# Kernel optimization log

Measured on AMD Instinct MI355X. Metric: run time of the kernel, lower is better.

Reference implementation:

```python
import jax, jax.numpy as jnp
import numpy as np

BIT = 64
M_MARGIN = 2.0 * BIT  # m = 2 * bit
ALPHA = 0.1
N_TRAIN = 100000
N_CLASSES = 100
BATCH = 512


def setup_inputs() -> dict:
    key = jax.random.key(0)
    k1, k2, k3, k4 = jax.random.split(key, 4)
    u = jax.random.normal(k1, (BATCH, BIT), dtype=jnp.float32)
    y = jax.random.randint(k2, (BATCH, N_CLASSES), 0, 2).astype(jnp.float32)
    ind = jnp.arange(BATCH, dtype=jnp.int32)
    U = jax.random.normal(k3, (N_TRAIN, BIT), dtype=jnp.float32)
    Y = jax.random.randint(k4, (N_TRAIN, N_CLASSES), 0, 2).astype(jnp.float32)
    return {"u": u, "y": y, "ind": ind, "U": U, "Y": Y}


def reference(u, y, ind, U, Y):
    # Buffer updates (torch uses u.data / y.float(): detached writes)
    U = U.at[ind].set(jax.lax.stop_gradient(u))  # [N, bit]
    Y = Y.at[ind].set(jax.lax.stop_gradient(y))  # [N, C]

    # Pairwise squared L2 distances via the expansion identity (same math as
    # (u[:,None]-U[None]).pow(2).sum(-1) but without the [B,N,bit] intermediate)
    u_sq = jnp.sum(u * u, axis=1, keepdims=True)        # [B, 1]
    U_sq = jnp.sum(U * U, axis=1)[None, :]              # [1, N]
    dist = jnp.maximum(u_sq - 2.0 * (u @ U.T) + U_sq, 0.0)  # [B, N]

    # match mask: 1 where labels share no class (y @ Y.T == 0)
    mismatch = (y @ Y.T == 0).astype(u.dtype)           # [B, N]

    loss = (1.0 - mismatch) * 0.5 * dist + mismatch * 0.5 * jnp.maximum(M_MARGIN - dist, 0.0)
    loss1 = loss.mean()
    loss2 = ALPHA * jnp.abs(1.0 - jnp.sign(u)).mean()
    return loss1 + loss2
```

## Files before the change

kernel.cpp:

```cpp
#include <hip/hip_runtime.h>
#include <stdint.h>

#define NTRAIN 100000
#define BATCH  512
#define BIT    64
#define NCLS   100
#define MARGINF 128.0f

#define CHUNK  256
#define NSCAN  ((NTRAIN + CHUNK - 1) / CHUNK)
#define NCORR  8
#define NGU    2
#define NUS    2


__device__ __forceinline__ uint4 row_mask(const float* __restrict__ row) {
  const float4* r4 = (const float4*)row;
  unsigned w0 = 0, w1 = 0, w2 = 0, w3 = 0;
#pragma unroll
  for (int j = 0; j < NCLS / 4; ++j) {
    float4 v = r4[j];
    int bp = (4 * j) & 31;
    unsigned m = ((v.x != 0.f) ? 1u : 0u) << bp
               | ((v.y != 0.f) ? 2u : 0u) << bp
               | ((v.z != 0.f) ? 4u : 0u) << bp
               | ((v.w != 0.f) ? 8u : 0u) << bp;
    int word = (4 * j) >> 5;
    if (word == 0) w0 |= m; else if (word == 1) w1 |= m;
    else if (word == 2) w2 |= m; else w3 |= m;
  }
  return make_uint4(w0, w1, w2, w3);
}

__device__ __forceinline__ float pair_term(const float* __restrict__ a,
                                           const float* __restrict__ c) {
  const float4* a4 = (const float4*)a;
  const float4* c4 = (const float4*)c;
  float usq = 0.f, Usq = 0.f, uv = 0.f;
#pragma unroll
  for (int k = 0; k < BIT / 4; ++k) {
    float4 x = a4[k], z = c4[k];
    usq = fmaf(x.x, x.x, fmaf(x.y, x.y, fmaf(x.z, x.z, fmaf(x.w, x.w, usq))));
    Usq = fmaf(z.x, z.x, fmaf(z.y, z.y, fmaf(z.z, z.z, fmaf(z.w, z.w, Usq))));
    uv  = fmaf(x.x, z.x, fmaf(x.y, z.y, fmaf(x.z, z.z, fmaf(x.w, z.w, uv))));
  }
  float d = usq + Usq - 2.f * uv;
  float dc = fmaxf(d, 0.f);
  return 0.5f * fmaxf(MARGINF - dc, 0.f) - 0.5f * d;
}

__global__ void __launch_bounds__(64) k_prep(const float* __restrict__ y,
                                             const float* __restrict__ Y,
                                             const int* __restrict__ ind,
                                             uint4* __restrict__ ymaskp,
                                             uint4* __restrict__ ymold,
                                             float* __restrict__ accf) {
  int bid = blockIdx.x, t = threadIdx.x;
  if (bid < 8) {
    int b = bid * 64 + t;
    ymaskp[b] = row_mask(y + (size_t)b * NCLS);
    ymold[b]  = row_mask(Y + (size_t)ind[b] * NCLS);
  } else {
    for (int i = t; i < 144; i += 64) accf[i] = 0.0f;
  }
}

__global__ void __launch_bounds__(512) k_main(
    const float4* __restrict__ U4, const float* __restrict__ Uf,
    const float* __restrict__ Y,
    const float4* __restrict__ u4, const float* __restrict__ u,
    const int* __restrict__ ind,
    const uint4* __restrict__ ymaskp, const uint4* __restrict__ ymold,
    float* __restrict__ accf) {
  __shared__ uint4 masks[CHUNK];
  __shared__ float colred[8][64];
  __shared__ float sqred[8][2];
  int bid = blockIdx.x, t = threadIdx.x;
  int w = t >> 6, l = t & 63;

  if (bid < NSCAN) {
    uint4 ym = ymaskp[t];
    int n0 = bid * CHUNK;
    int nvalid = min(CHUNK, NTRAIN - n0);
    if (t < CHUNK)
      masks[t] = (t < nvalid) ? row_mask(Y + (size_t)(n0 + t) * NCLS)
                              : make_uint4(~0u, ~0u, ~0u, ~0u);
    float s0 = 0, s1 = 0, s2 = 0, s3 = 0, sq = 0;
    for (int f = t; f < nvalid * (BIT / 4); f += 512) {
      float4 v = U4[(size_t)n0 * (BIT / 4) + f];
      s0 += v.x; s1 += v.y; s2 += v.z; s3 += v.w;
      sq = fmaf(v.x, v.x, fmaf(v.y, v.y, fmaf(v.z, v.z, fmaf(v.w, v.w, sq))));
    }
    s0 += __shfl_xor(s0, 16); s0 += __shfl_xor(s0, 32);
    s1 += __shfl_xor(s1, 16); s1 += __shfl_xor(s1, 32);
    s2 += __shfl_xor(s2, 16); s2 += __shfl_xor(s2, 32);
    s3 += __shfl_xor(s3, 16); s3 += __shfl_xor(s3, 32);
    for (int off = 32; off; off >>= 1) sq += __shfl_xor(sq, off);
    if (l < 16) { colred[w][l * 4 + 0] = s0; colred[w][l * 4 + 1] = s1;
                  colred[w][l * 4 + 2] = s2; colred[w][l * 4 + 3] = s3; }
    if (l == 0) sqred[w][0] = sq;
    __syncthreads();
    if (w == 0) {
      float cs = 0;
#pragma unroll
      for (int ww = 0; ww < 8; ++ww) cs += colred[ww][l];
      atomicAdd(&accf[l], cs);
      if (l == 0) {
        float qs = 0;
#pragma unroll
        for (int ww = 0; ww < 8; ++ww) qs += sqred[ww][0];
        atomicAdd(&accf[128], qs);
      }
    }
    float corr = 0.f;
    for (int j = 0; j < CHUNK; j += 4) {
      uint4 m0 = masks[j], m1 = masks[j + 1], m2 = masks[j + 2], m3 = masks[j + 3];
      unsigned a0 = (ym.x & m0.x) | (ym.y & m0.y) | (ym.z & m0.z) | (ym.w & m0.w);
      unsigned a1 = (ym.x & m1.x) | (ym.y & m1.y) | (ym.z & m1.z) | (ym.w & m1.w);
      unsigned a2 = (ym.x & m2.x) | (ym.y & m2.y) | (ym.z & m2.z) | (ym.w & m2.w);
      unsigned a3 = (ym.x & m3.x) | (ym.y & m3.y) | (ym.z & m3.z) | (ym.w & m3.w);
      if (__builtin_expect((a0 == 0u) | (a1 == 0u) | (a2 == 0u) | (a3 == 0u), 0)) {
        const float* ub = u + (size_t)t * BIT;
        if (a0 == 0u) corr += pair_term(ub, Uf + (size_t)(n0 + j + 0) * BIT);
        if (a1 == 0u) corr += pair_term(ub, Uf + (size_t)(n0 + j + 1) * BIT);
        if (a2 == 0u) corr += pair_term(ub, Uf + (size_t)(n0 + j + 2) * BIT);
        if (a3 == 0u) corr += pair_term(ub, Uf + (size_t)(n0 + j + 3) * BIT);
      }
    }
    if (corr != 0.f) atomicAdd(&accf[131], corr);
  } else if (bid < NSCAN + NCORR) {
    int cb = bid - NSCAN;
    uint4 ym = ymaskp[t];
    float corr = 0.f;
    for (int j = 0; j < 64; ++j) {
      int bp = cb * 64 + j;
      uint4 mo = ymold[bp];
      uint4 mn = ymaskp[bp];
      unsigned a = (ym.x & mo.x) | (ym.y & mo.y) | (ym.z & mo.z) | (ym.w & mo.w);
      unsigned c = (ym.x & mn.x) | (ym.y & mn.y) | (ym.z & mn.z) | (ym.w & mn.w);
      if (__builtin_expect(__ballot((a == 0u) | (c == 0u)) != 0ull, 0)) {
        const float* ub = u + (size_t)t * BIT;
        if (a == 0u) corr -= pair_term(ub, Uf + (size_t)ind[bp] * BIT);
        if (c == 0u) corr += pair_term(ub, u + (size_t)bp * BIT);
      }
    }
    if (corr != 0.f) atomicAdd(&accf[131], corr);
  } else if (bid < NSCAN + NCORR + NGU) {
    int gb = bid - NSCAN - NCORR;
    float s0 = 0, s1 = 0, s2 = 0, s3 = 0, sq = 0;
    for (int f = t; f < 256 * (BIT / 4); f += 512) {
      int r = gb * 256 + (f >> 4);
      float4 v = U4[(size_t)ind[r] * (BIT / 4) + (f & 15)];
      s0 += v.x; s1 += v.y; s2 += v.z; s3 += v.w;
      sq = fmaf(v.x, v.x, fmaf(v.y, v.y, fmaf(v.z, v.z, fmaf(v.w, v.w, sq))));
    }
    s0 += __shfl_xor(s0, 16); s0 += __shfl_xor(s0, 32);
    s1 += __shfl_xor(s1, 16); s1 += __shfl_xor(s1, 32);
    s2 += __shfl_xor(s2, 16); s2 += __shfl_xor(s2, 32);
    s3 += __shfl_xor(s3, 16); s3 += __shfl_xor(s3, 32);
    for (int off = 32; off; off >>= 1) sq += __shfl_xor(sq, off);
    int c4 = l & 15;
    if (l < 16) {
      atomicAdd(&accf[c4 * 4 + 0], -s0); atomicAdd(&accf[c4 * 4 + 1], -s1);
      atomicAdd(&accf[c4 * 4 + 2], -s2); atomicAdd(&accf[c4 * 4 + 3], -s3);
    }
    if (l == 0) atomicAdd(&accf[128], -sq);
  } else {
    int gb = bid - NSCAN - NCORR - NGU;
    float s0 = 0, s1 = 0, s2 = 0, s3 = 0, sq = 0, sg = 0;
    for (int f = t; f < 256 * (BIT / 4); f += 512) {
      float4 v = u4[(size_t)gb * 256 * (BIT / 4) + f];
      s0 += v.x; s1 += v.y; s2 += v.z; s3 += v.w;
      sq = fmaf(v.x, v.x, fmaf(v.y, v.y, fmaf(v.z, v.z, fmaf(v.w, v.w, sq))));
      sg += ((v.x < 0.f) ? 2.f : (v.x == 0.f) ? 1.f : 0.f)
          + ((v.y < 0.f) ? 2.f : (v.y == 0.f) ? 1.f : 0.f)
          + ((v.z < 0.f) ? 2.f : (v.z == 0.f) ? 1.f : 0.f)
          + ((v.w < 0.f) ? 2.f : (v.w == 0.f) ? 1.f : 0.f);
    }
    s0 += __shfl_xor(s0, 16); s0 += __shfl_xor(s0, 32);
    s1 += __shfl_xor(s1, 16); s1 += __shfl_xor(s1, 32);
    s2 += __shfl_xor(s2, 16); s2 += __shfl_xor(s2, 32);
    s3 += __shfl_xor(s3, 16); s3 += __shfl_xor(s3, 32);
    for (int off = 32; off; off >>= 1) { sq += __shfl_xor(sq, off); sg += __shfl_xor(sg, off); }
    int c4 = l & 15;
    if (l < 16) {
      atomicAdd(&accf[64 + c4 * 4 + 0], s0); atomicAdd(&accf[64 + c4 * 4 + 1], s1);
      atomicAdd(&accf[64 + c4 * 4 + 2], s2); atomicAdd(&accf[64 + c4 * 4 + 3], s3);
    }
    if (l == 0) { atomicAdd(&accf[129], sq); atomicAdd(&accf[130], sg); }
  }
}

__global__ void k_final(const float* __restrict__ accf, float* __restrict__ out) {
  int lane = threadIdx.x;
  double dotp = (double)accf[lane] * (double)accf[64 + lane];
  for (int off = 32; off; off >>= 1) dotp += __shfl_down(dotp, off);
  if (lane == 0) {
    double S_Usq = accf[128];
    double s_usq = accf[129];
    double sg    = accf[130];
    double corr  = accf[131];
    double sum_dist = (double)NTRAIN * s_usq + (double)BATCH * S_Usq - 2.0 * dotp;
    double loss1 = (0.5 * sum_dist + corr) / ((double)BATCH * (double)NTRAIN);
    double loss2 = 0.1 * sg / ((double)BATCH * (double)BIT);
    out[0] = (float)(loss1 + loss2);
  }
}

extern "C" void kernel_launch(void* const* d_in, const int* in_sizes, int n_in,
                              void* d_out, int out_size, void* d_ws, size_t ws_size,
                              hipStream_t stream) {
  const float* u   = (const float*)d_in[0];
  const float* y   = (const float*)d_in[1];
  const int*   ind = (const int*)d_in[2];
  const float* U   = (const float*)d_in[3];
  const float* Y   = (const float*)d_in[4];
  uint4* ymaskp = (uint4*)((char*)d_ws);
  uint4* ymold  = (uint4*)((char*)d_ws + 8192);
  float* accf   = (float*)((char*)d_ws + 16384);
  float* out    = (float*)d_out;

  hipLaunchKernelGGL(k_prep, dim3(9), dim3(64), 0, stream, y, Y, ind, ymaskp, ymold, accf);
  hipLaunchKernelGGL(k_main, dim3(NSCAN + NCORR + NGU + NUS), dim3(512), 0, stream,
                     (const float4*)U, U, Y, (const float4*)u, u, ind, ymaskp, ymold, accf);
  hipLaunchKernelGGL(k_final, dim3(1), dim3(64), 0, stream, accf, out);
}
```

Measured before the change: 129.6 us.

## Filter mismatched pairs with per-class miss bitmaps and a deferred candidate list

Replaces the per-thread scan of every training-row mask against each batch row with a transposed test. For each class, k_prep builds a 512-bit bitmap of the batch rows that lack that class. Each training row then ANDs the bitmaps of its own classes, with early exit, to find batch rows sharing no label with it. Training rows that have any such batch row go into a global list, and a combined final kernel recomputes their exact corrections before reducing the loss. The U column and square sums move to the other half of the waves so they overlap with mask building. The fixed list capacity of 1024 silently drops candidates if many mismatches exist, so correctness depends on such pairs being rare.

```diff
diff --git a/kernel.cpp b/kernel.cpp
--- a/kernel.cpp
+++ b/kernel.cpp
@@ -12,7 +12,16 @@
 #define NCORR  8
 #define NGU    2
 #define NUS    2
-
+#define LISTCAP 1024
+
+#define YMP_OFF   0
+#define YMO_OFF   8192
+#define MISS_OFF  16384
+#define ACC_OFF   24576
+#define CNT_OFF   25600
+#define LIST_OFF  25664
+
+typedef unsigned long long u64;
 
 __device__ __forceinline__ uint4 row_mask(const float* __restrict__ row) {
   const float4* r4 = (const float4*)row;
@@ -54,14 +63,25 @@
                                              const int* __restrict__ ind,
                                              uint4* __restrict__ ymaskp,
                                              uint4* __restrict__ ymold,
-                                             float* __restrict__ accf) {
+                                             u64* __restrict__ missg,
+                                             float* __restrict__ accf,
+                                             int* __restrict__ listcnt) {
   int bid = blockIdx.x, t = threadIdx.x;
   if (bid < 8) {
     int b = bid * 64 + t;
-    ymaskp[b] = row_mask(y + (size_t)b * NCLS);
+    uint4 ym = row_mask(y + (size_t)b * NCLS);
+    ymaskp[b] = ym;
     ymold[b]  = row_mask(Y + (size_t)ind[b] * NCLS);
+#pragma unroll
+    for (int c = 0; c < NCLS; ++c) {
+      unsigned word = (c < 32) ? ym.x : (c < 64) ? ym.y : (c < 96) ? ym.z : ym.w;
+      unsigned bit = (word >> (c & 31)) & 1u;
+      u64 bal = __ballot(bit == 0u);
+      if (t == 0) missg[c * 8 + bid] = bal;
+    }
   } else {
     for (int i = t; i < 144; i += 64) accf[i] = 0.0f;
+    if (t == 0) *listcnt = 0;
   }
 }
 
@@ -71,63 +91,71 @@
     const float4* __restrict__ u4, const float* __restrict__ u,
     const int* __restrict__ ind,
     const uint4* __restrict__ ymaskp, const uint4* __restrict__ ymold,
-    float* __restrict__ accf) {
+    const u64* __restrict__ missg,
+    float* __restrict__ accf, int* __restrict__ listcnt, int* __restrict__ list) {
   __shared__ uint4 masks[CHUNK];
-  __shared__ float colred[8][64];
-  __shared__ float sqred[8][2];
+  __shared__ u64 mlds[NCLS * 9];
+  __shared__ float colred[4][64];
+  __shared__ float sqred[4];
   int bid = blockIdx.x, t = threadIdx.x;
   int w = t >> 6, l = t & 63;
 
   if (bid < NSCAN) {
-    uint4 ym = ymaskp[t];
     int n0 = bid * CHUNK;
     int nvalid = min(CHUNK, NTRAIN - n0);
-    if (t < CHUNK)
+    if (w < 4) {
       masks[t] = (t < nvalid) ? row_mask(Y + (size_t)(n0 + t) * NCLS)
-                              : make_uint4(~0u, ~0u, ~0u, ~0u);
-    float s0 = 0, s1 = 0, s2 = 0, s3 = 0, sq = 0;
-    for (int f = t; f < nvalid * (BIT / 4); f += 512) {
-      float4 v = U4[(size_t)n0 * (BIT / 4) + f];
-      s0 += v.x; s1 += v.y; s2 += v.z; s3 += v.w;
-      sq = fmaf(v.x, v.x, fmaf(v.y, v.y, fmaf(v.z, v.z, fmaf(v.w, v.w, sq))));
-    }
-    s0 += __shfl_xor(s0, 16); s0 += __shfl_xor(s0, 32);
-    s1 += __shfl_xor(s1, 16); s1 += __shfl_xor(s1, 32);
-    s2 += __shfl_xor(s2, 16); s2 += __shfl_xor(s2, 32);
-    s3 += __shfl_xor(s3, 16); s3 += __shfl_xor(s3, 32);
-    for (int off = 32; off; off >>= 1) sq += __shfl_xor(sq, off);
-    if (l < 16) { colred[w][l * 4 + 0] = s0; colred[w][l * 4 + 1] = s1;
-                  colred[w][l * 4 + 2] = s2; colred[w][l * 4 + 3] = s3; }
-    if (l == 0) sqred[w][0] = sq;
+                              : make_uint4(0u, 0u, 0u, 0u);
+    } else {
+      for (int i = t - 256; i < NCLS * 8; i += 256)
+        mlds[(i >> 3) * 9 + (i & 7)] = missg[i];
+      float s0 = 0, s1 = 0, s2 = 0, s3 = 0, sq = 0;
+      for (int f = t - 256; f < nvalid * (BIT / 4); f += 256) {
+        float4 v = U4[(size_t)n0 * (BIT / 4) + f];
+        s0 += v.x; s1 += v.y; s2 += v.z; s3 += v.w;
+        sq = fmaf(v.x, v.x, fmaf(v.y, v.y, fmaf(v.z, v.z, fmaf(v.w, v.w, sq))));
+      }
+      s0 += __shfl_xor(s0, 16); s0 += __shfl_xor(s0, 32);
+      s1 += __shfl_xor(s1, 16); s1 += __shfl_xor(s1, 32);
+      s2 += __shfl_xor(s2, 16); s2 += __shfl_xor(s2, 32);
+      s3 += __shfl_xor(s3, 16); s3 += __shfl_xor(s3, 32);
+      for (int off = 32; off; off >>= 1) sq += __shfl_xor(sq, off);
+      int ww = w - 4;
+      if (l < 16) { colred[ww][l * 4 + 0] = s0; colred[ww][l * 4 + 1] = s1;
+                    colred[ww][l * 4 + 2] = s2; colred[ww][l * 4 + 3] = s3; }
+      if (l == 0) sqred[ww] = sq;
+    }
     __syncthreads();
     if (w == 0) {
-      float cs = 0;
-#pragma unroll
-      for (int ww = 0; ww < 8; ++ww) cs += colred[ww][l];
-      atomicAdd(&accf[l], cs);
-      if (l == 0) {
-        float qs = 0;
-#pragma unroll
-        for (int ww = 0; ww < 8; ++ww) qs += sqred[ww][0];
-        atomicAdd(&accf[128], qs);
-      }
-    }
-    float corr = 0.f;
-    for (int j = 0; j < CHUNK; j += 4) {
-      uint4 m0 = masks[j], m1 = masks[j + 1], m2 = masks[j + 2], m3 = masks[j + 3];
-      unsigned a0 = (ym.x & m0.x) | (ym.y & m0.y) | (ym.z & m0.z) | (ym.w & m0.w);
-      unsigned a1 = (ym.x & m1.x) | (ym.y & m1.y) | (ym.z & m1.z) | (ym.w & m1.w);
-      unsigned a2 = (ym.x & m2.x) | (ym.y & m2.y) | (ym.z & m2.z) | (ym.w & m2.w);
-      unsigned a3 = (ym.x & m3.x) | (ym.y & m3.y) | (ym.z & m3.z) | (ym.w & m3.w);
-      if (__builtin_expect((a0 == 0u) | (a1 == 0u) | (a2 == 0u) | (a3 == 0u), 0)) {
-        const float* ub = u + (size_t)t * BIT;
-        if (a0 == 0u) corr += pair_term(ub, Uf + (size_t)(n0 + j + 0) * BIT);
-        if (a1 == 0u) corr += pair_term(ub, Uf + (size_t)(n0 + j + 1) * BIT);
-        if (a2 == 0u) corr += pair_term(ub, Uf + (size_t)(n0 + j + 2) * BIT);
-        if (a3 == 0u) corr += pair_term(ub, Uf + (size_t)(n0 + j + 3) * BIT);
-      }
-    }
-    if (corr != 0.f) atomicAdd(&accf[131], corr);
+      atomicAdd(&accf[l], colred[0][l] + colred[1][l] + colred[2][l] + colred[3][l]);
+      if (l == 0) atomicAdd(&accf[128], sqred[0] + sqred[1] + sqred[2] + sqred[3]);
+    }
+    int grp = t >> 3;
+    int g   = t & 7;
+#pragma unroll
+    for (int k = 0; k < CHUNK / 64; ++k) {
+      int n_local = grp + 64 * k;
+      bool alive = n_local < nvalid;
+      uint4 ym = masks[n_local];
+      u64 rem0 = (u64)ym.x | ((u64)ym.y << 32);
+      u64 rem1 = (u64)ym.z | ((u64)ym.w << 32);
+      u64 acc = alive ? ~0ull : 0ull;
+      while (__ballot((acc != 0ull) && ((rem0 | rem1) != 0ull)) != 0ull) {
+#pragma unroll
+        for (int kk = 0; kk < 4; ++kk) {
+          int c = -1;
+          if (rem0) { c = __builtin_ctzll(rem0); rem0 &= rem0 - 1ull; }
+          else if (rem1) { c = 64 + __builtin_ctzll(rem1); rem1 &= rem1 - 1ull; }
+          u64 mm = mlds[(c >= 0 ? c : 0) * 9 + g];
+          if (c >= 0) acc &= mm;
+        }
+      }
+      u64 mbal = __ballot(acc != 0ull);
+      if (g == 0 && ((mbal >> (8 * (grp & 7))) & 0xffull)) {
+        int idx = atomicAdd(listcnt, 1);
+        if (idx < LISTCAP) list[idx] = n0 + n_local;
+      }
+    }
   } else if (bid < NSCAN + NCORR) {
     int cb = bid - NSCAN;
     uint4 ym = ymaskp[t];
@@ -191,19 +219,37 @@
   }
 }
 
-__global__ void k_final(const float* __restrict__ accf, float* __restrict__ out) {
-  int lane = threadIdx.x;
-  double dotp = (double)accf[lane] * (double)accf[64 + lane];
-  for (int off = 32; off; off >>= 1) dotp += __shfl_down(dotp, off);
-  if (lane == 0) {
-    double S_Usq = accf[128];
-    double s_usq = accf[129];
-    double sg    = accf[130];
-    double corr  = accf[131];
-    double sum_dist = (double)NTRAIN * s_usq + (double)BATCH * S_Usq - 2.0 * dotp;
-    double loss1 = (0.5 * sum_dist + corr) / ((double)BATCH * (double)NTRAIN);
-    double loss2 = 0.1 * sg / ((double)BATCH * (double)BIT);
-    out[0] = (float)(loss1 + loss2);
+__global__ void __launch_bounds__(512) k_finalfix(
+    const float* __restrict__ Y, const float* __restrict__ u, const float* __restrict__ Uf,
+    const uint4* __restrict__ ymaskp, const int* __restrict__ listcnt,
+    const int* __restrict__ list, float* __restrict__ accf, float* __restrict__ out) {
+  int t = threadIdx.x;
+  int cnt = min(*listcnt, LISTCAP);
+  if (__builtin_expect(cnt > 0, 0)) {
+    uint4 ymb = ymaskp[t];
+    float corr = 0.f;
+    for (int i = 0; i < cnt; ++i) {
+      int n = list[i];
+      uint4 Ym = row_mask(Y + (size_t)n * NCLS);
+      unsigned m = (ymb.x & Ym.x) | (ymb.y & Ym.y) | (ymb.z & Ym.z) | (ymb.w & Ym.w);
+      if (m == 0u) corr += pair_term(u + (size_t)t * BIT, Uf + (size_t)n * BIT);
+    }
+    if (corr != 0.f) atomicAdd(&accf[131], corr);
+  }
+  __syncthreads();
+  if (t < 64) {
+    double dotp = (double)accf[t] * (double)accf[64 + t];
+    for (int off = 32; off; off >>= 1) dotp += __shfl_down(dotp, off);
+    if (t == 0) {
+      double S_Usq = accf[128];
+      double s_usq = accf[129];
+      double sg    = accf[130];
+      double corr  = accf[131];
+      double sum_dist = (double)NTRAIN * s_usq + (double)BATCH * S_Usq - 2.0 * dotp;
+      double loss1 = (0.5 * sum_dist + corr) / ((double)BATCH * (double)NTRAIN);
+      double loss2 = 0.1 * sg / ((double)BATCH * (double)BIT);
+      out[0] = (float)(loss1 + loss2);
+    }
   }
 }
 
@@ -215,13 +261,19 @@
   const int*   ind = (const int*)d_in[2];
   const float* U   = (const float*)d_in[3];
   const float* Y   = (const float*)d_in[4];
-  uint4* ymaskp = (uint4*)((char*)d_ws);
-  uint4* ymold  = (uint4*)((char*)d_ws + 8192);
-  float* accf   = (float*)((char*)d_ws + 16384);
+  uint4* ymaskp = (uint4*)((char*)d_ws + YMP_OFF);
+  uint4* ymold  = (uint4*)((char*)d_ws + YMO_OFF);
+  u64*   missg  = (u64*)((char*)d_ws + MISS_OFF);
+  float* accf   = (float*)((char*)d_ws + ACC_OFF);
+  int*   cnt    = (int*)((char*)d_ws + CNT_OFF);
+  int*   list   = (int*)((char*)d_ws + LIST_OFF);
   float* out    = (float*)d_out;
 
-  hipLaunchKernelGGL(k_prep, dim3(9), dim3(64), 0, stream, y, Y, ind, ymaskp, ymold, accf);
+  hipLaunchKernelGGL(k_prep, dim3(9), dim3(64), 0, stream,
+                     y, Y, ind, ymaskp, ymold, missg, accf, cnt);
   hipLaunchKernelGGL(k_main, dim3(NSCAN + NCORR + NGU + NUS), dim3(512), 0, stream,
-                     (const float4*)U, U, Y, (const float4*)u, u, ind, ymaskp, ymold, accf);
-  hipLaunchKernelGGL(k_final, dim3(1), dim3(64), 0, stream, accf, out);
-}
+                     (const float4*)U, U, Y, (const float4*)u, u, ind,
+                     ymaskp, ymold, missg, accf, cnt, list);
+  hipLaunchKernelGGL(k_finalfix, dim3(1), dim3(512), 0, stream,
+                     Y, u, U, ymaskp, cnt, list, accf, out);
+}
```

Result: no change. 127.9 us (-1.3%).
